# Kernel tuning notes

Measured on AMD Instinct MI355X. Metric: run time of the kernel, lower is better.

## Reference

```python
import jax, jax.numpy as jnp
import numpy as np


def _ln(z, g, b):
    m = z.mean(-1, keepdims=True)
    v = ((z - m) ** 2).mean(-1, keepdims=True)
    return (z - m) * jax.lax.rsqrt(v + 1e-5) * g + b


def _pe(T, D):
    # standard sinusoidal positional encoding (T, D)
    pos = np.arange(T)[:, None]
    i = np.arange(D // 2)[None, :]
    ang = pos / np.power(10000.0, 2.0 * i / D)
    pe = np.zeros((T, D), dtype=np.float32)
    pe[:, 0::2] = np.sin(ang)
    pe[:, 1::2] = np.cos(ang)
    return jnp.asarray(pe)


def _whconv(z, Hinc, filt, W, b):
    # Wavelet hypergraph convolution: psi diag(filt) psi^{-1} Z W + b
    # psi = heat-kernel wavelet of normalized hypergraph Laplacian, 2nd-order Taylor (K=2, s=1)
    S = Hinc.shape[0]
    Dv = Hinc.sum(1) + 1e-6          # node degrees
    De = Hinc.sum(0) + 1e-6          # hyperedge degrees
    Hn = Hinc * (Dv ** -0.5)[:, None]
    A = (Hn / De[None, :]) @ Hn.T    # Dv^-1/2 H De^-1 H^T Dv^-1/2
    I = jnp.eye(S, dtype=z.dtype)
    L = I - A
    L2 = 0.5 * (L @ L)
    psi = I - L + L2                  # exp(-L) approx
    psi_inv = I + L + L2              # exp(+L) approx
    return psi @ (filt[:, None] * (psi_inv @ z)) @ W + b


def setup_inputs():
    S, T, F, D, NS, E, K = 2048, 64, 16, 256, 4, 128, 32
    key = jax.random.key(0)
    ks = iter(jax.random.split(key, 64))
    nrm = lambda shp: jax.random.normal(next(ks), shp, jnp.float32) * 0.02
    return dict(
        x=jax.random.normal(next(ks), (S, T, F), jnp.float32),
        snapshot=(jax.random.uniform(next(ks), (NS, S, E)) < 0.05).astype(jnp.float32),
        params_snapshot=jax.random.uniform(next(ks), (NS,), jnp.float32, 0.0, 0.99),
        beta=jnp.array([0.33, 0.33, 0.33], jnp.float32),
        W_emb=nrm((F, D)), b_emb=jnp.zeros((D,), jnp.float32),
        Wq=nrm((D, D)), bq=jnp.zeros((D,), jnp.float32),
        Wk=nrm((D, D)), bk=jnp.zeros((D,), jnp.float32),
        Wv=nrm((D, D)), bv=jnp.zeros((D,), jnp.float32),
        Wo=nrm((D, D)), bo=jnp.zeros((D,), jnp.float32),
        ln1_g=jnp.ones((D,), jnp.float32), ln1_b=jnp.zeros((D,), jnp.float32),
        W_int=nrm((D, D)), b_int=jnp.zeros((D,), jnp.float32),
        W_mix=nrm((2 * D, D)), b_mix=jnp.zeros((D,), jnp.float32),
        ln2_g=jnp.ones((D,), jnp.float32), ln2_b=jnp.zeros((D,), jnp.float32),
        Wt=nrm((D, D)), bt=jnp.zeros((D,), jnp.float32), vt=nrm((D,)),
        Wh1=nrm((D, D)), bh1=jnp.zeros((D,), jnp.float32), filt1=jnp.ones((S,), jnp.float32),
        Wh2=nrm((D, D)), bh2=jnp.zeros((D,), jnp.float32), filt2=jnp.ones((S,), jnp.float32),
        Wa=nrm((D, D)), Wb=nrm((D, D)), Wg=nrm((D, D)), bg=jnp.zeros((D,), jnp.float32),
        Wm1=nrm((D, D)), bm1=jnp.zeros((D,), jnp.float32),
        Wm2=nrm((D, 1)), bm2=jnp.zeros((1,), jnp.float32),
        num_edges=K,
    )


def reference(x, snapshot, params_snapshot, beta, W_emb, b_emb, Wq, bq, Wk, bk, Wv, bv,
              Wo, bo, ln1_g, ln1_b, W_int, b_int, W_mix, b_mix, ln2_g, ln2_b,
              Wt, bt, vt, Wh1, bh1, filt1, Wh2, bh2, filt2, Wa, Wb, Wg, bg,
              Wm1, bm1, Wm2, bm2, num_edges):
    S, T, _ = x.shape
    D = W_emb.shape[1]
    H = 8
    dh = D // H
    # feature embedding + positional encoding
    h = x @ W_emb + b_emb + _pe(T, D)
    # intra-stock (per-stock temporal) multi-head self-attention + residual + LN
    q = (h @ Wq + bq).reshape(S, T, H, dh)
    k = (h @ Wk + bk).reshape(S, T, H, dh)
    v = (h @ Wv + bv).reshape(S, T, H, dh)
    att = jax.nn.softmax(jnp.einsum('sqhd,skhd->shqk', q, k) / jnp.sqrt(jnp.float32(dh)), axis=-1)
    o = jnp.einsum('shqk,skhd->sqhd', att, v).reshape(S, T, D) @ Wo + bo
    h = _ln(h + o, ln1_g, ln1_b)
    # intensity function + mixing layer (Linear -> ReLU -> LayerNorm)
    intensity = jax.nn.softplus(h @ W_int + b_int)
    z = jax.nn.relu(jnp.concatenate([h, intensity], axis=-1) @ W_mix + b_mix)
    h = _ln(z, ln2_g, ln2_b)
    # temporal attention pooling: (S,T,D) -> (S,D)
    u = jnp.tanh(h @ Wt + bt)
    a = jax.nn.softmax(u @ vt, axis=-1)          # (S,T)
    xs = jnp.einsum('st,std->sd', a, h)           # (S,D)
    # per-snapshot two-layer wavelet hypergraph conv (dropout = eval identity)
    def per_snap(Hinc):
        r1 = jax.nn.leaky_relu(_whconv(xs, Hinc, filt1, Wh1, bh1), 0.1)
        return _whconv(r1, Hinc, filt2, Wh2, bh2)
    reps = jax.vmap(per_snap)(snapshot)           # (NS,S,D)
    hyper = jnp.einsum('n,nsd->sd', params_snapshot, reps)
    # dynamic graph learning: top-k learned similarity graph
    sim = (xs @ Wa) @ (xs @ Wb).T / jnp.sqrt(jnp.float32(D))
    kth = jax.lax.top_k(sim, num_edges)[0][:, -1]
    Adyn = jax.nn.softmax(jnp.where(sim >= kth[:, None], sim, -jnp.inf), axis=-1)
    dyn = jax.nn.relu(Adyn @ xs @ Wg + bg)
    # fusion ('sum' mode) + MLP head
    w = jax.nn.softmax(beta)
    fused = w[0] * xs + w[1] * dyn + w[2] * hyper
    return jax.nn.relu(fused @ Wm1 + bm1) @ Wm2 + bm2   # (S,1)
```

## Files before the change

### kernel.cpp

```cpp
#include <hip/hip_runtime.h>
#include <math.h>

#define S_ 2048
#define T_ 64
#define F_ 16
#define D_ 256
#define NS_ 4
#define E_ 128
#define H_ 8
#define KC_ 32
#define SD_ (S_*D_)
#define HS 260

#define PK_ATT 0
#define PK_WO  393216
#define PK_WI  524288
#define PK_WT  655360
#define PK_WM  786432
#define PKBASE 11674112

typedef __attribute__((ext_vector_type(8))) short bf16x8;
typedef __attribute__((ext_vector_type(4))) float f32x4;

__device__ __forceinline__ float warp_sum64(float v){
  #pragma unroll
  for (int o=32;o>=1;o>>=1) v += __shfl_xor(v,o);
  return v;
}
__device__ __forceinline__ float warp_max64(float v){
  #pragma unroll
  for (int o=32;o>=1;o>>=1) v = fmaxf(v,__shfl_xor(v,o));
  return v;
}
__device__ __forceinline__ float softplus_f(float v){
  return fmaxf(v,0.f) + log1pf(__expf(-fabsf(v)));
}
__device__ __forceinline__ float tanh_f(float v){
  float t = __expf(-2.f*fabsf(v));
  float r = (1.f-t)/(1.f+t);
  return copysignf(r, v);
}
__device__ __forceinline__ void splitf(float f, short& h, short& l){
  unsigned u = __float_as_uint(f);
  unsigned hb = (u + 0x7FFFu + ((u>>16)&1u)) >> 16;
  float fl = f - __uint_as_float(hb<<16);
  unsigned v = __float_as_uint(fl);
  unsigned lb = (v + 0x7FFFu + ((v>>16)&1u)) >> 16;
  h = (short)hb; l = (short)lb;
}
__device__ __forceinline__ f32x4 mfma3(bf16x8 ah, bf16x8 al, bf16x8 bh, bf16x8 bl, f32x4 c){
  c = __builtin_amdgcn_mfma_f32_16x16x32_bf16(al, bh, c, 0,0,0);
  c = __builtin_amdgcn_mfma_f32_16x16x32_bf16(ah, bl, c, 0,0,0);
  c = __builtin_amdgcn_mfma_f32_16x16x32_bf16(ah, bh, c, 0,0,0);
  return c;
}
__device__ __forceinline__ void afrag_f32(const float* base, int stride, int rbase, int ks, int lane, bf16x8& hi, bf16x8& lo){
  const float* p = base + (rbase + (lane&15))*stride + ks + ((lane>>4)<<3);
  #pragma unroll
  for (int jj=0;jj<8;++jj){ short h,l; splitf(p[jj],h,l); hi[jj]=h; lo[jj]=l; }
}
__device__ __forceinline__ void bfrag_pk(const unsigned* pk, int tile, int lane, bf16x8& hi, bf16x8& lo){
  const unsigned* p = pk + (((tile<<6) + lane)<<3);
  #pragma unroll
  for (int jj=0;jj<8;++jj){ unsigned u=p[jj]; hi[jj]=(short)(u & 0xffffu); lo[jj]=(short)(u>>16); }
}

__global__ void pack_qkv(const float* __restrict__ W, short* __restrict__ dst, int vplane){
  int i = blockIdx.x*256 + threadIdx.x;
  int jj=i&7, n=(i>>3)&15, q=(i>>7)&3, ntg=(i>>9)&15, kt=i>>13;
  float f = W[(kt*32 + q*8 + jj)*256 + (ntg*16+n)];
  short h,l; splitf(f,h,l);
  int hp = ntg>>2, ntl = ntg&3;
  int base = ((hp*8+kt)*6 + vplane*2)*2048;
  int local = ntl*512 + (q*16+n)*8 + jj;
  dst[base+local] = h;
  dst[base+2048+local] = l;
}
__global__ void pack_post(const float* __restrict__ W, short* __restrict__ dst){
  int i = blockIdx.x*256 + threadIdx.x;
  int jj=i&7, n=(i>>3)&15, q=(i>>7)&3, ntg=(i>>9)&15, kt=i>>13;
  float f = W[(kt*32 + q*8 + jj)*256 + (ntg*16+n)];
  short h,l; splitf(f,h,l);
  int dl = kt*16384 + ntg*512 + (q*16+n)*8 + jj;
  dst[dl] = h;
  dst[dl+8192] = l;
}

__global__ void pe_kernel(float* __restrict__ pe){
  int i = blockIdx.x*256 + threadIdx.x;
  int t = i >> 8, d = i & 255;
  int ii = d >> 1;
  float w = __expf(-(float)ii * (logf(10000.f)/128.f));
  float ang = (float)t * w;
  pe[i] = (d & 1) ? cosf(ang) : sinf(ang);
}

__launch_bounds__(512,1)
__global__ void stageA_kernel(
    const float* __restrict__ x, const float* __restrict__ pe,
    const float* __restrict__ Wemb, const float* __restrict__ bemb,
    const float* __restrict__ bq, const float* __restrict__ bk, const float* __restrict__ bv,
    const float* __restrict__ bo,
    const float* __restrict__ ln1g, const float* __restrict__ ln1b,
    const float* __restrict__ bint,
    const float* __restrict__ bmix,
    const float* __restrict__ ln2g, const float* __restrict__ ln2b,
    const float* __restrict__ bt,
    const float* __restrict__ vt,
    const short* __restrict__ pkc,
    float* __restrict__ xs)
{
  __shared__ float hbuf[T_][HS];
  __shared__ __attribute__((aligned(16))) char smem[85504];

  short*    wst   = (short*)smem;
  unsigned* k2f2  = (unsigned*)smem;
  unsigned* v2f2  = (unsigned*)(smem + 16384);
  float*    qb2   = (float*)(smem + 32768);
  float*    scb2  = (float*)(smem + 50176);
  float*    smallb= (float*)(smem + 84992);

  const int j  = threadIdx.x;
  const int s  = blockIdx.x;
  const int w  = j >> 6;
  const int lane = j & 63;
  const int m_ = lane & 15, qd = lane >> 4;
  const int rg2 = w >> 1, par = w & 1;
  const int rbase = rg2*16;
  const int rv = w*8;
  const int c0 = lane;

  {
    float* xb = (float*)smem;
    const float* xp = x + (long)s*T_*F_;
    for (int i=j; i<T_*F_; i+=512) xb[i] = xp[i];
  }
  __syncthreads();

  {
    const float* xb = (const float*)smem;
    float acc[8][4];
    #pragma unroll
    for (int r=0;r<8;++r){acc[r][0]=0;acc[r][1]=0;acc[r][2]=0;acc[r][3]=0;}
    #pragma unroll
    for (int k=0;k<F_;++k){
      float w0=Wemb[k*D_+c0], w1=Wemb[k*D_+c0+64], w2=Wemb[k*D_+c0+128], w3=Wemb[k*D_+c0+192];
      #pragma unroll
      for (int r=0;r<8;++r){
        float hv = xb[(rv+r)*F_+k];
        acc[r][0]+=hv*w0; acc[r][1]+=hv*w1; acc[r][2]+=hv*w2; acc[r][3]+=hv*w3;
      }
    }
    float b0=bemb[c0],b1=bemb[c0+64],b2=bemb[c0+128],b3=bemb[c0+192];
    #pragma unroll
    for (int r=0;r<8;++r){
      int t = rv+r;
      hbuf[t][c0]     = acc[r][0]+b0+pe[t*D_+c0];
      hbuf[t][c0+64]  = acc[r][1]+b1+pe[t*D_+c0+64];
      hbuf[t][c0+128] = acc[r][2]+b2+pe[t*D_+c0+128];
      hbuf[t][c0+192] = acc[r][3]+b3+pe[t*D_+c0+192];
    }
  }
  __syncthreads();

  bf16x8 AH[8], AL[8];
  #pragma unroll
  for (int kt=0;kt<8;++kt) afrag_f32(&hbuf[0][0], HS, rbase, kt*32, lane, AH[kt], AL[kt]);

  const float rs = 0.17677669529663687f;
  f32x4 co[8];
  #pragma unroll
  for (int t=0;t<8;++t) co[t] = (f32x4){0.f,0.f,0.f,0.f};

  for (int hp=0; hp<4; ++hp){
    f32x4 qa[2],ka[2],va[2];
    #pragma unroll
    for (int t=0;t<2;++t){
      qa[t]=(f32x4){0.f,0.f,0.f,0.f};
      ka[t]=(f32x4){0.f,0.f,0.f,0.f};
      va[t]=(f32x4){0.f,0.f,0.f,0.f};
    }
    bf16x8 pre[3];
    {
      const short* b0 = pkc + PK_ATT + (hp*8)*12288;
      #pragma unroll
      for (int r=0;r<3;++r) pre[r] = *(const bf16x8*)(b0 + (j+r*512)*8);
    }
    for (int kt=0; kt<8; ++kt){
      __syncthreads();
      #pragma unroll
      for (int r=0;r<3;++r) *(bf16x8*)(wst + (j+r*512)*8) = pre[r];
      __syncthreads();
      if (kt<7){
        const short* nb = pkc + PK_ATT + (hp*8+kt+1)*12288;
        #pragma unroll
        for (int r=0;r<3;++r) pre[r] = *(const bf16x8*)(nb + (j+r*512)*8);
      }
      bf16x8 ah = AH[kt], al = AL[kt];
      #pragma unroll
      for (int t=0;t<2;++t){
        int ntl = par*2+t;
        bf16x8 bh,bl;
        bh = *(bf16x8*)(wst +         ntl*512 + lane*8);
        bl = *(bf16x8*)(wst + 2048  + ntl*512 + lane*8);
        qa[t]=mfma3(ah,al,bh,bl,qa[t]);
        bh = *(bf16x8*)(wst + 4096  + ntl*512 + lane*8);
        bl = *(bf16x8*)(wst + 6144  + ntl*512 + lane*8);
        ka[t]=mfma3(ah,al,bh,bl,ka[t]);
        bh = *(bf16x8*)(wst + 8192  + ntl*512 + lane*8);
        bl = *(bf16x8*)(wst + 10240 + ntl*512 + lane*8);
        va[t]=mfma3(ah,al,bh,bl,va[t]);
      }
    }
    __syncthreads();
    #pragma unroll
    for (int t=0;t<2;++t){
      int ntg = par*2+t;
      #pragma unroll
      for (int r=0;r<4;++r){
        int trow = rbase + qd*4 + r;
        int pcp = ntg*16 + m_;
        int head = pcp >> 5;
        int cp = pcp & 31;
        int col = hp*64 + pcp;
        qb2[trow*68 + pcp] = (qa[t][r] + bq[col]) * rs;
        short hS,lS;
        float kv2 = ka[t][r] + bk[col];
        splitf(kv2,hS,lS);
        k2f2[head*2048 + (((trow>>4)*4 + (cp>>3))*16 + (trow&15))*8 + (cp&7)]
            = (unsigned)(unsigned short)hS | ((unsigned)(unsigned short)lS<<16);
        float vv2 = va[t][r] + bv[col];
        splitf(vv2,hS,lS);
        v2f2[head*2048 + ((((trow>>5)*2 + (cp>>4))*4 + ((trow>>3)&3))*16 + (cp&15))*8 + (trow&7)]
            = (unsigned)(unsigned short)hS | ((unsigned)(unsigned short)lS<<16);
      }
    }
    __syncthreads();
    float* scb = scb2 + par*4352;
    {
      bf16x8 ah,al;
      afrag_f32(qb2, 68, rbase, par*32, lane, ah, al);
      f32x4 sc4[4];
      #pragma unroll
      for (int nt=0;nt<4;++nt){
        bf16x8 bh,bl; bfrag_pk(k2f2 + par*2048, nt, lane, bh, bl);
        sc4[nt] = mfma3(ah,al,bh,bl,(f32x4){0.f,0.f,0.f,0.f});
      }
      #pragma unroll
      for (int r=0;r<4;++r){
        float mx = fmaxf(fmaxf(sc4[0][r],sc4[1][r]),fmaxf(sc4[2][r],sc4[3][r]));
        #pragma unroll
        for (int o=8;o>=1;o>>=1) mx = fmaxf(mx, __shfl_xor(mx,o));
        float es = 0.f;
        #pragma unroll
        for (int nt=0;nt<4;++nt){ float e=__expf(sc4[nt][r]-mx); sc4[nt][r]=e; es+=e; }
        #pragma unroll
        for (int o=8;o>=1;o>>=1) es += __shfl_xor(es,o);
        float inv = 1.f/es;
        int trow = rbase + qd*4 + r;
        #pragma unroll
        for (int nt=0;nt<4;++nt) scb[trow*68 + nt*16 + m_] = sc4[nt][r]*inv;
      }
    }
    {
      f32x4 oa[2];
      oa[0]=(f32x4){0.f,0.f,0.f,0.f}; oa[1]=(f32x4){0.f,0.f,0.f,0.f};
      #pragma unroll
      for (int kt=0;kt<2;++kt){
        bf16x8 ah2,al2; afrag_f32(scb, 68, rbase, kt*32, lane, ah2, al2);
        #pragma unroll
        for (int nt=0;nt<2;++nt){
          bf16x8 bh,bl; bfrag_pk(v2f2 + par*2048, kt*2+nt, lane, bh, bl);
          oa[nt]=mfma3(ah2,al2,bh,bl,oa[nt]);
        }
      }
      #pragma unroll
      for (int nt=0;nt<2;++nt){
        #pragma unroll
        for (int r=0;r<4;++r)
          qb2[(rbase+qd*4+r)*68 + par*32 + nt*16 + m_] = oa[nt][r];
      }
    }
    for (int ks=0; ks<2; ++ks){
      bf16x8 preo[4];
      {
        const short* wob = pkc + PK_WO + (hp*2+ks)*16384;
        #pragma unroll
        for (int r=0;r<4;++r) preo[r] = *(const bf16x8*)(wob + (j+r*512)*8);
      }
      __syncthreads();
      #pragma unroll
      for (int r=0;r<4;++r) *(bf16x8*)(wst + (j+r*512)*8) = preo[r];
      __syncthreads();
      bf16x8 ah,al; afrag_f32(qb2, 68, rbase, ks*32, lane, ah, al);
      #pragma unroll
      for (int t=0;t<8;++t){
        int ntg = 2*t+par;
        bf16x8 bh = *(bf16x8*)(wst +        ntg*512 + lane*8);
        bf16x8 bl = *(bf16x8*)(wst + 8192 + ntg*512 + lane*8);
        co[t]=mfma3(ah,al,bh,bl,co[t]);
      }
    }
  }

  #pragma unroll
  for (int t=0;t<8;++t){
    int cc = (2*t+par)*16+m_;
    float bov = bo[cc];
    #pragma unroll
    for (int r=0;r<4;++r)
      hbuf[rbase+qd*4+r][cc] += co[t][r] + bov;
  }
  __syncthreads();

  {
    float g0=ln1g[c0],g1=ln1g[c0+64],g2=ln1g[c0+128],g3=ln1g[c0+192];
    float bb0=ln1b[c0],bb1=ln1b[c0+64],bb2=ln1b[c0+128],bb3=ln1b[c0+192];
    for (int rr=0;rr<8;++rr){
      int t=rv+rr;
      float v0=hbuf[t][c0],v1=hbuf[t][c0+64],v2=hbuf[t][c0+128],v3=hbuf[t][c0+192];
      float sm=warp_sum64(v0+v1+v2+v3);
      float sq=warp_sum64(v0*v0+v1*v1+v2*v2+v3*v3);
      float mean=sm*(1.f/256.f);
      float inv=rsqrtf(fmaxf(sq*(1.f/256.f)-mean*mean,0.f)+1e-5f);
      hbuf[t][c0]    =(v0-mean)*inv*g0+bb0;
      hbuf[t][c0+64] =(v1-mean)*inv*g1+bb1;
      hbuf[t][c0+128]=(v2-mean)*inv*g2+bb2;
      hbuf[t][c0+192]=(v3-mean)*inv*g3+bb3;
    }
  }
  __syncthreads();

  f32x4 az[8];
  #pragma unroll
  for (int t=0;t<8;++t) az[t]=(f32x4){0.f,0.f,0.f,0.f};
  {
    bf16x8 prew[4];
    #pragma unroll
    for (int r=0;r<4;++r) prew[r] = *(const bf16x8*)(pkc + PK_WM + (j+r*512)*8);
    for (int kt=0; kt<8; ++kt){
      __syncthreads();
      #pragma unroll
      for (int r=0;r<4;++r) *(bf16x8*)(wst + (j+r*512)*8) = prew[r];
      __syncthreads();
      if (kt<7){
        const short* nb = pkc + PK_WM + (kt+1)*16384;
        #pragma unroll
        for (int r=0;r<4;++r) prew[r] = *(const bf16x8*)(nb + (j+r*512)*8);
      }
      bf16x8 ah,al; afrag_f32(&hbuf[0][0], HS, rbase, kt*32, lane, ah, al);
      #pragma unroll
      for (int t=0;t<8;++t){
        int ntg = 2*t+par;
        bf16x8 bh = *(bf16x8*)(wst +        ntg*512 + lane*8);
        bf16x8 bl = *(bf16x8*)(wst + 8192 + ntg*512 + lane*8);
        az[t]=mfma3(ah,al,bh,bl,az[t]);
      }
    }
  }

  {
    f32x4 ai[8];
    #pragma unroll
    for (int t=0;t<8;++t) ai[t]=(f32x4){0.f,0.f,0.f,0.f};
    bf16x8 prew[4];
    #pragma unroll
    for (int r=0;r<4;++r) prew[r] = *(const bf16x8*)(pkc + PK_WI + (j+r*512)*8);
    for (int kt=0; kt<8; ++kt){
      __syncthreads();
      #pragma unroll
      for (int r=0;r<4;++r) *(bf16x8*)(wst + (j+r*512)*8) = prew[r];
      __syncthreads();
      if (kt<7){
        const short* nb = pkc + PK_WI + (kt+1)*16384;
        #pragma unroll
        for (int r=0;r<4;++r) prew[r] = *(const bf16x8*)(nb + (j+r*512)*8);
      }
      bf16x8 ah,al; afrag_f32(&hbuf[0][0], HS, rbase, kt*32, lane, ah, al);
      #pragma unroll
      for (int t=0;t<8;++t){
        int ntg = 2*t+par;
        bf16x8 bh = *(bf16x8*)(wst +        ntg*512 + lane*8);
        bf16x8 bl = *(bf16x8*)(wst + 8192 + ntg*512 + lane*8);
        ai[t]=mfma3(ah,al,bh,bl,ai[t]);
      }
    }
    __syncthreads();
    #pragma unroll
    for (int t=0;t<8;++t){
      int cc = (2*t+par)*16+m_;
      float bb = bint[cc];
      #pragma unroll
      for (int r=0;r<4;++r)
        hbuf[rbase+qd*4+r][cc] = softplus_f(ai[t][r]+bb);
    }
  }

  {
    bf16x8 prew[4];
    #pragma unroll
    for (int r=0;r<4;++r) prew[r] = *(const bf16x8*)(pkc + PK_WM + 8*16384 + (j+r*512)*8);
    for (int kt=0; kt<8; ++kt){
      __syncthreads();
      #pragma unroll
      for (int r=0;r<4;++r) *(bf16x8*)(wst + (j+r*512)*8) = prew[r];
      __syncthreads();
      if (kt<7){
        const short* nb = pkc + PK_WM + (9+kt)*16384;
        #pragma unroll
        for (int r=0;r<4;++r) prew[r] = *(const bf16x8*)(nb + (j+r*512)*8);
      }
      bf16x8 ah,al; afrag_f32(&hbuf[0][0], HS, rbase, kt*32, lane, ah, al);
      #pragma unroll
      for (int t=0;t<8;++t){
        int ntg = 2*t+par;
        bf16x8 bh = *(bf16x8*)(wst +        ntg*512 + lane*8);
        bf16x8 bl = *(bf16x8*)(wst + 8192 + ntg*512 + lane*8);
        az[t]=mfma3(ah,al,bh,bl,az[t]);
      }
    }
  }
  __syncthreads();
  #pragma unroll
  for (int t=0;t<8;++t){
    int cc = (2*t+par)*16+m_;
    float bb = bmix[cc];
    #pragma unroll
    for (int r=0;r<4;++r)
      hbuf[rbase+qd*4+r][cc] = fmaxf(az[t][r]+bb,0.f);
  }
  __syncthreads();

  {
    float g0=ln2g[c0],g1=ln2g[c0+64],g2=ln2g[c0+128],g3=ln2g[c0+192];
    float bb0=ln2b[c0],bb1=ln2b[c0+64],bb2=ln2b[c0+128],bb3=ln2b[c0+192];
    for (int rr=0;rr<8;++rr){
      int t=rv+rr;
      float v0=hbuf[t][c0],v1=hbuf[t][c0+64],v2=hbuf[t][c0+128],v3=hbuf[t][c0+192];
      float sm=warp_sum64(v0+v1+v2+v3);
      float sq=warp_sum64(v0*v0+v1*v1+v2*v2+v3*v3);
      float mean=sm*(1.f/256.f);
      float inv=rsqrtf(fmaxf(sq*(1.f/256.f)-mean*mean,0.f)+1e-5f);
      hbuf[t][c0]    =(v0-mean)*inv*g0+bb0;
      hbuf[t][c0+64] =(v1-mean)*inv*g1+bb1;
      hbuf[t][c0+128]=(v2-mean)*inv*g2+bb2;
      hbuf[t][c0+192]=(v3-mean)*inv*g3+bb3;
    }
  }

  {
    f32x4 at4[8];
    #pragma unroll
    for (int t=0;t<8;++t) at4[t]=(f32x4){0.f,0.f,0.f,0.f};
    bf16x8 prew[4];
    #pragma unroll
    for (int r=0;r<4;++r) prew[r] = *(const bf16x8*)(pkc + PK_WT + (j+r*512)*8);
    for (int kt=0; kt<8; ++kt){
      __syncthreads();
      #pragma unroll
      for (int r=0;r<4;++r) *(bf16x8*)(wst + (j+r*512)*8) = prew[r];
      __syncthreads();
      if (kt<7){
        const short* nb = pkc + PK_WT + (kt+1)*16384;
        #pragma unroll
        for (int r=0;r<4;++r) prew[r] = *(const bf16x8*)(nb + (j+r*512)*8);
      }
      bf16x8 ah,al; afrag_f32(&hbuf[0][0], HS, rbase, kt*32, lane, ah, al);
      #pragma unroll
      for (int t=0;t<8;++t){
        int ntg = 2*t+par;
        bf16x8 bh = *(bf16x8*)(wst +        ntg*512 + lane*8);
        bf16x8 bl = *(bf16x8*)(wst + 8192 + ntg*512 + lane*8);
        at4[t]=mfma3(ah,al,bh,bl,at4[t]);
      }
    }
    float pr[4] = {0.f,0.f,0.f,0.f};
    #pragma unroll
    for (int t=0;t<8;++t){
      int cc = (2*t+par)*16+m_;
      float btc = bt[cc], vtc = vt[cc];
      #pragma unroll
      for (int r=0;r<4;++r) pr[r] += tanh_f(at4[t][r]+btc)*vtc;
    }
    #pragma unroll
    for (int r=0;r<4;++r){
      float p = pr[r];
      p += __shfl_xor(p,1); p += __shfl_xor(p,2);
      p += __shfl_xor(p,4); p += __shfl_xor(p,8);
      if (m_==0) smallb[par*64 + rbase + qd*4 + r] = p;
    }
  }
  __syncthreads();
  if (j < 64){
    float v = smallb[j] + smallb[64+j];
    float m = warp_max64(v);
    float e = __expf(v-m);
    float ssum = warp_sum64(e);
    smallb[64+j] = e/ssum;
  }
  __syncthreads();
  if (j < 256){
    float acc=0.f;
    #pragma unroll 8
    for (int t=0;t<T_;++t) acc += smallb[64+t]*hbuf[t][j];
    xs[(long)s*D_+j] = acc;
  }
}

__global__ void hg_deg(const float* __restrict__ Hinc, float* __restrict__ Dv, float* __restrict__ De){
  const int n = blockIdx.y, s0 = blockIdx.x*64;
  const float* Hp = Hinc + (long)n*S_*E_;
  const int j = threadIdx.x;
  {
    int r = j>>2, q = j&3;
    const float* rp = Hp + (long)(s0+r)*E_ + q*32;
    float sm=0;
    #pragma unroll
    for (int e=0;e<32;++e) sm += rp[e];
    sm += __shfl_xor(sm,1); sm += __shfl_xor(sm,2);
    if (q==0) Dv[n*S_+s0+r]=sm+1e-6f;
  }
  if (j < E_){
    float cs=0;
    for (int ss=0;ss<64;++ss) cs += Hp[(long)(s0+ss)*E_+j];
    atomicAdd(&De[n*E_+j], cs);
  }
}

__global__ void hg_scale(const float* __restrict__ Hinc, const float* __restrict__ Dv,
                         const float* __restrict__ De, float* __restrict__ Hn, float* __restrict__ HnD){
  long i = (long)blockIdx.x*256+threadIdx.x;
  int n = (int)(i >> 18);
  int rem = (int)(i & 262143);
  int srow = rem >> 7;
  int e = rem & 127;
  float h = Hinc[i];
  float hn = h * rsqrtf(Dv[n*S_+srow]);
  Hn[i] = hn;
  HnD[i] = hn / (De[n*E_+e]+1e-6f);
}

__launch_bounds__(256,1)
__global__ void hg_phase1(const float* __restrict__ Hn, const float* __restrict__ M,
                          long mz, float* __restrict__ Ppart)
{
  __shared__ float hl[64*E_];
  __shared__ float ml[64*128];
  const int kc = blockIdx.x, dh = blockIdx.y, n = blockIdx.z;
  const int j = threadIdx.x;
  const float* Hp = Hn + ((long)n*S_ + (long)kc*64)*E_;
  const float* Mp = M + (long)n*mz + (long)kc*64*D_ + dh*128;
  for (int i=j*4; i<64*E_; i+=1024) *(float4*)&hl[i] = *(const float4*)&Hp[i];
  for (int i=j*4; i<64*128; i+=1024){
    int row = i>>7, cc = i&127;
    *(float4*)&ml[i] = *(const float4*)&Mp[(long)row*D_ + cc];
  }
  __syncthreads();
  const int eg = j & 15, dg = j >> 4;
  float acc[8][8];
  #pragma unroll
  for (int e=0;e<8;++e){
    #pragma unroll
    for (int d=0;d<8;++d) acc[e][d]=0.f;
  }
  for (int ss=0; ss<64; ++ss){
    float hv[8], mv[8];
    *(float4*)&hv[0] = *(const float4*)&hl[ss*E_+eg*8];
    *(float4*)&hv[4] = *(const float4*)&hl[ss*E_+eg*8+4];
    *(float4*)&mv[0] = *(const float4*)&ml[ss*128+dg*8];
    *(float4*)&mv[4] = *(const float4*)&ml[ss*128+dg*8+4];
    #pragma unroll
    for (int e=0;e<8;++e){
      #pragma unroll
      for (int d=0;d<8;++d) acc[e][d] += hv[e]*mv[d];
    }
  }
  float* Pp = Ppart + (long)(n*KC_+kc)*E_*D_ + dh*128;
  #pragma unroll
  for (int e=0;e<8;++e){
    int erow = eg*8+e;
    #pragma unroll
    for (int d4=0;d4<8;d4+=4){
      float4 v = make_float4(acc[e][d4],acc[e][d4+1],acc[e][d4+2],acc[e][d4+3]);
      *(float4*)&Pp[(long)erow*D_ + dg*8 + d4] = v;
    }
  }
}

__global__ void hg_reduceP(const float* __restrict__ Ppart, float* __restrict__ P){
  const int n = blockIdx.y;
  int base = blockIdx.x*1024;
  for (int i = base + threadIdx.x; i < base+1024; i += 256){
    const float* pp = Ppart + (long)n*KC_*E_*D_ + i;
    float a = 0;
    #pragma unroll
    for (int kc=0;kc<KC_;++kc) a += pp[(long)kc*E_*D_];
    P[(long)n*E_*D_ + i] = a;
  }
}

__launch_bounds__(256,1)
__global__ void hg_phase2(const float* __restrict__ HnD, const float* __restrict__ P,
                          const float* __restrict__ X1, long x1z, float c1,
                          const float* __restrict__ X2, long x2z, float c2,
                          float c3, const float* __restrict__ filt, int usefilt,
                          float* __restrict__ out)
{
  __shared__ float al[E_*68];
  __shared__ float pl[E_*68];
  const int st = blockIdx.x*64, dt = blockIdx.y*64, n = blockIdx.z;
  const int j = threadIdx.x;
  {
    const int r = j >> 2, k0 = (j&3)*32;
    const float* hp = HnD + ((long)n*S_ + st + r)*E_ + k0;
    #pragma unroll
    for (int kk=0; kk<32; kk+=4){
      float4 v = *(const float4*)&hp[kk];
      al[(k0+kk+0)*68+r]=v.x;
      al[(k0+kk+1)*68+r]=v.y;
      al[(k0+kk+2)*68+r]=v.z;
      al[(k0+kk+3)*68+r]=v.w;
    }
  }
  for (int idx=j; idx<E_*16; idx+=256){
    int k = idx>>4, dsub = (idx&15)*4;
    *(float4*)&pl[k*68+dsub] = *(const float4*)&P[((long)n*E_+k)*D_ + dt + dsub];
  }
  __syncthreads();
  const int tx = j&15, ty = j>>4;
  float acc[4][4];
  #pragma unroll
  for (int i=0;i<4;++i){acc[i][0]=0;acc[i][1]=0;acc[i][2]=0;acc[i][3]=0;}
  for (int k=0;k<E_;++k){
    float4 a = *(const float4*)&al[k*68+ty*4];
    float4 b = *(const float4*)&pl[k*68+tx*4];
    acc[0][0]+=a.x*b.x; acc[0][1]+=a.x*b.y; acc[0][2]+=a.x*b.z; acc[0][3]+=a.x*b.w;
    acc[1][0]+=a.y*b.x; acc[1][1]+=a.y*b.y; acc[1][2]+=a.y*b.z; acc[1][3]+=a.y*b.w;
    acc[2][0]+=a.z*b.x; acc[2][1]+=a.z*b.y; acc[2][2]+=a.z*b.z; acc[2][3]+=a.z*b.w;
    acc[3][0]+=a.w*b.x; acc[3][1]+=a.w*b.y; acc[3][2]+=a.w*b.z; acc[3][3]+=a.w*b.w;
  }
  #pragma unroll
  for (int i=0;i<4;++i){
    int srow = st + ty*4 + i;
    float f = usefilt ? filt[srow] : 1.f;
    #pragma unroll
    for (int m=0;m<4;++m){
      int d = dt + tx*4+m;
      long li = (long)srow*D_ + d;
      float v = c3*acc[i][m];
      if (X1) v += c1*X1[x1z*n + li];
      if (X2) v += c2*X2[x2z*n + li];
      out[((long)n*S_ + srow)*D_ + d] = f*v;
    }
  }
}

__launch_bounds__(256,1)
__global__ void gemm_nn(const float* __restrict__ A, long az,
                        const float* __restrict__ B, long bz,
                        float* __restrict__ C, long cz,
                        int K, int N,
                        const float* __restrict__ bias, int act)
{
  __shared__ float al[32*68];
  __shared__ float bl[32*68];
  const int mt = blockIdx.x*64, nt = blockIdx.y*64, zz = blockIdx.z;
  const int j = threadIdx.x;
  const float* Ap = A + (long)az*zz;
  const float* Bp = B + (long)bz*zz;
  const int tx = j&15, ty = j>>4;
  float acc[4][4];
  #pragma unroll
  for (int i=0;i<4;++i){acc[i][0]=0;acc[i][1]=0;acc[i][2]=0;acc[i][3]=0;}
  for (int k0=0;k0<K;k0+=32){
    #pragma unroll
    for (int half=0; half<2; ++half){
      int idx = j + half*256;
      int r = idx>>3, kk=(idx&7)*4;
      float4 v = *(const float4*)&Ap[(long)(mt+r)*K + k0+kk];
      al[(kk+0)*68+r]=v.x; al[(kk+1)*68+r]=v.y; al[(kk+2)*68+r]=v.z; al[(kk+3)*68+r]=v.w;
    }
    #pragma unroll
    for (int half=0; half<2; ++half){
      int idx = j + half*256;
      int r = idx>>4, cc=(idx&15)*4;
      *(float4*)&bl[r*68+cc] = *(const float4*)&Bp[(long)(k0+r)*N + nt+cc];
    }
    __syncthreads();
    #pragma unroll
    for (int kk=0;kk<32;++kk){
      float4 a = *(const float4*)&al[kk*68+ty*4];
      float4 b = *(const float4*)&bl[kk*68+tx*4];
      acc[0][0]+=a.x*b.x; acc[0][1]+=a.x*b.y; acc[0][2]+=a.x*b.z; acc[0][3]+=a.x*b.w;
      acc[1][0]+=a.y*b.x; acc[1][1]+=a.y*b.y; acc[1][2]+=a.y*b.z; acc[1][3]+=a.y*b.w;
      acc[2][0]+=a.z*b.x; acc[2][1]+=a.z*b.y; acc[2][2]+=a.z*b.z; acc[2][3]+=a.z*b.w;
      acc[3][0]+=a.w*b.x; acc[3][1]+=a.w*b.y; acc[3][2]+=a.w*b.z; acc[3][3]+=a.w*b.w;
    }
    __syncthreads();
  }
  #pragma unroll
  for (int i=0;i<4;++i){
    int row = mt+ty*4+i;
    #pragma unroll
    for (int m=0;m<4;++m){
      int col = nt+tx*4+m;
      float v = acc[i][m];
      if (bias) v += bias[col];
      if (act==1) v = fmaxf(v,0.f);
      else if (act==2) v = (v>0.f)? v : 0.1f*v;
      C[(long)cz*zz + (long)row*N + col] = v;
    }
  }
}

__launch_bounds__(256,1)
__global__ void gemm_nt_scaled(const float* __restrict__ A, const float* __restrict__ B,
                               float* __restrict__ C, int K, float scale)
{
  __shared__ float al[32*68];
  __shared__ float bl[32*68];
  const int mt = blockIdx.x*64, nt = blockIdx.y*64;
  const int j = threadIdx.x;
  const int tx = j&15, ty = j>>4;
  float acc[4][4];
  #pragma unroll
  for (int i=0;i<4;++i){acc[i][0]=0;acc[i][1]=0;acc[i][2]=0;acc[i][3]=0;}
  for (int k0=0;k0<K;k0+=32){
    #pragma unroll
    for (int half=0; half<2; ++half){
      int idx = j + half*256;
      int r = idx>>3, kk=(idx&7)*4;
      float4 v = *(const float4*)&A[(long)(mt+r)*K + k0+kk];
      al[(kk+0)*68+r]=v.x; al[(kk+1)*68+r]=v.y; al[(kk+2)*68+r]=v.z; al[(kk+3)*68+r]=v.w;
    }
    #pragma unroll
    for (int half=0; half<2; ++half){
      int idx = j + half*256;
      int r = idx>>3, kk=(idx&7)*4;
      float4 v = *(const float4*)&B[(long)(nt+r)*K + k0+kk];
      bl[(kk+0)*68+r]=v.x; bl[(kk+1)*68+r]=v.y; bl[(kk+2)*68+r]=v.z; bl[(kk+3)*68+r]=v.w;
    }
    __syncthreads();
    #pragma unroll
    for (int kk=0;kk<32;++kk){
      float4 a = *(const float4*)&al[kk*68+ty*4];
      float4 b = *(const float4*)&bl[kk*68+tx*4];
      acc[0][0]+=a.x*b.x; acc[0][1]+=a.x*b.y; acc[0][2]+=a.x*b.z; acc[0][3]+=a.x*b.w;
      acc[1][0]+=a.y*b.x; acc[1][1]+=a.y*b.y; acc[1][2]+=a.y*b.z; acc[1][3]+=a.y*b.w;
      acc[2][0]+=a.z*b.x; acc[2][1]+=a.z*b.y; acc[2][2]+=a.z*b.z; acc[2][3]+=a.z*b.w;
      acc[3][0]+=a.w*b.x; acc[3][1]+=a.w*b.y; acc[3][2]+=a.w*b.z; acc[3][3]+=a.w*b.w;
    }
    __syncthreads();
  }
  #pragma unroll
  for (int i=0;i<4;++i){
    #pragma unroll
    for (int m=0;m<4;++m){
      C[(long)(mt+ty*4+i)*S_ + nt+tx*4+m] = acc[i][m]*scale;
    }
  }
}

__launch_bounds__(256,1)
__global__ void topk_gather(const float* __restrict__ sim, const float* __restrict__ xs,
                            const int* __restrict__ Kp, float* __restrict__ dynpre)
{
  __shared__ float row[S_];
  __shared__ float work[S_];
  __shared__ float wred[4]; __shared__ int ired[4];
  __shared__ float selw[256]; __shared__ int seli[256];
  __shared__ int cnt; __shared__ float sh_kth, sh_max, sh_den;
  const int s = blockIdx.x, j = threadIdx.x;
  const float* rp = sim + (long)s*S_;
  for (int i=j;i<S_;i+=256){ float v=rp[i]; row[i]=v; work[i]=v; }
  if (j==0) cnt=0;
  __syncthreads();
  const int K = Kp[0];
  for (int it=0; it<K; ++it){
    float m=-3.0e38f; int mi=0;
    for (int i=j;i<S_;i+=256){ float v=work[i]; if (v>m){m=v;mi=i;} }
    #pragma unroll
    for (int o=32;o>=1;o>>=1){
      float om=__shfl_xor(m,o); int oi=__shfl_xor(mi,o);
      if (om>m){m=om;mi=oi;}
    }
    if ((j&63)==0){ wred[j>>6]=m; ired[j>>6]=mi; }
    __syncthreads();
    if (j==0){
      float bm=wred[0]; int bi=ired[0];
      #pragma unroll
      for (int w=1;w<4;++w) if (wred[w]>bm){bm=wred[w];bi=ired[w];}
      work[bi]=-3.0e38f;
      if (it==0) sh_max=bm;
      sh_kth=bm;
    }
    __syncthreads();
  }
  const float kth=sh_kth, rmax=sh_max;
  for (int i=j;i<S_;i+=256){
    float v=row[i];
    if (v>=kth){
      int p=atomicAdd(&cnt,1);
      if (p<256){ seli[p]=i; selw[p]=__expf(v-rmax); }
    }
  }
  __syncthreads();
  int c = cnt; if (c>256) c=256;
// ... 147 lines not shown
```

Measured before the change: 1.459 ms.

## Store activations as split bf16 planes and stream weights directly from global

The activation buffer moves from fp32 in LDS to pre-split hi/lo bf16 planes, so MFMA A-fragments become single vector loads instead of per-element splitting. The post-LN GEMMs are restructured so each wave owns two output column tiles across all 64 rows, with B fragments loaded straight from global memory and register double-buffered across the W_mix, W_int and W_t GEMMs. This removes the per-k-step LDS weight staging and its two barriers, and the Wo GEMM also reads weights directly from global. The cost is more global/L2 traffic per wave and a split/recombine step on every elementwise read-modify-write of activations, with a small precision change from the double-bf16 storage.

```diff
diff --git a/kernel.cpp b/kernel.cpp
--- a/kernel.cpp
+++ b/kernel.cpp
@@ -10,7 +10,7 @@
 #define H_ 8
 #define KC_ 32
 #define SD_ (S_*D_)
-#define HS 260
+#define PS 264
 
 #define PK_ATT 0
 #define PK_WO  393216
@@ -59,10 +59,22 @@
   #pragma unroll
   for (int jj=0;jj<8;++jj){ short h,l; splitf(p[jj],h,l); hi[jj]=h; lo[jj]=l; }
 }
+__device__ __forceinline__ bf16x8 afrag_pk(const short* plane, int rbase, int ks, int lane){
+  return *(const bf16x8*)(plane + (rbase + (lane&15))*PS + ks + ((lane>>4)<<3));
+}
 __device__ __forceinline__ void bfrag_pk(const unsigned* pk, int tile, int lane, bf16x8& hi, bf16x8& lo){
   const unsigned* p = pk + (((tile<<6) + lane)<<3);
   #pragma unroll
   for (int jj=0;jj<8;++jj){ unsigned u=p[jj]; hi[jj]=(short)(u & 0xffffu); lo[jj]=(short)(u>>16); }
+}
+__device__ __forceinline__ void store_h(short* Hh, short* Hl, int r, int c, float f){
+  short h,l; splitf(f,h,l);
+  Hh[r*PS+c]=h; Hl[r*PS+c]=l;
+}
+__device__ __forceinline__ float load_h(const short* Hh, const short* Hl, int r, int c){
+  int idx=r*PS+c;
+  return __uint_as_float(((unsigned)(unsigned short)Hh[idx])<<16)
+       + __uint_as_float(((unsigned)(unsigned short)Hl[idx])<<16);
 }
 
 __global__ void pack_qkv(const float* __restrict__ W, short* __restrict__ dst, int vplane){
@@ -110,7 +122,8 @@
     const short* __restrict__ pkc,
     float* __restrict__ xs)
 {
-  __shared__ float hbuf[T_][HS];
+  __shared__ __attribute__((aligned(16))) short hbh[64*PS];
+  __shared__ __attribute__((aligned(16))) short hbl[64*PS];
   __shared__ __attribute__((aligned(16))) char smem[85504];
 
   short*    wst   = (short*)smem;
@@ -118,7 +131,7 @@
   unsigned* v2f2  = (unsigned*)(smem + 16384);
   float*    qb2   = (float*)(smem + 32768);
   float*    scb2  = (float*)(smem + 50176);
-  float*    smallb= (float*)(smem + 84992);
+  float*    poolb = (float*)smem;
 
   const int j  = threadIdx.x;
   const int s  = blockIdx.x;
@@ -152,20 +165,24 @@
       }
     }
     float b0=bemb[c0],b1=bemb[c0+64],b2=bemb[c0+128],b3=bemb[c0+192];
+    __syncthreads();
     #pragma unroll
     for (int r=0;r<8;++r){
       int t = rv+r;
-      hbuf[t][c0]     = acc[r][0]+b0+pe[t*D_+c0];
-      hbuf[t][c0+64]  = acc[r][1]+b1+pe[t*D_+c0+64];
-      hbuf[t][c0+128] = acc[r][2]+b2+pe[t*D_+c0+128];
-      hbuf[t][c0+192] = acc[r][3]+b3+pe[t*D_+c0+192];
+      store_h(hbh,hbl,t,c0,     acc[r][0]+b0+pe[t*D_+c0]);
+      store_h(hbh,hbl,t,c0+64,  acc[r][1]+b1+pe[t*D_+c0+64]);
+      store_h(hbh,hbl,t,c0+128, acc[r][2]+b2+pe[t*D_+c0+128]);
+      store_h(hbh,hbl,t,c0+192, acc[r][3]+b3+pe[t*D_+c0+192]);
     }
   }
   __syncthreads();
 
   bf16x8 AH[8], AL[8];
   #pragma unroll
-  for (int kt=0;kt<8;++kt) afrag_f32(&hbuf[0][0], HS, rbase, kt*32, lane, AH[kt], AL[kt]);
+  for (int kt=0;kt<8;++kt){
+    AH[kt] = afrag_pk(hbh, rbase, kt*32, lane);
+    AL[kt] = afrag_pk(hbl, rbase, kt*32, lane);
+  }
 
   const float rs = 0.17677669529663687f;
   f32x4 co[8];
@@ -281,23 +298,15 @@
           qb2[(rbase+qd*4+r)*68 + par*32 + nt*16 + m_] = oa[nt][r];
       }
     }
+    __syncthreads();
     for (int ks=0; ks<2; ++ks){
-      bf16x8 preo[4];
-      {
-        const short* wob = pkc + PK_WO + (hp*2+ks)*16384;
-        #pragma unroll
-        for (int r=0;r<4;++r) preo[r] = *(const bf16x8*)(wob + (j+r*512)*8);
-      }
-      __syncthreads();
-      #pragma unroll
-      for (int r=0;r<4;++r) *(bf16x8*)(wst + (j+r*512)*8) = preo[r];
-      __syncthreads();
       bf16x8 ah,al; afrag_f32(qb2, 68, rbase, ks*32, lane, ah, al);
+      const short* wob = pkc + PK_WO + (hp*2+ks)*16384 + lane*8;
       #pragma unroll
       for (int t=0;t<8;++t){
         int ntg = 2*t+par;
-        bf16x8 bh = *(bf16x8*)(wst +        ntg*512 + lane*8);
-        bf16x8 bl = *(bf16x8*)(wst + 8192 + ntg*512 + lane*8);
+        bf16x8 bh = *(const bf16x8*)(wob + ntg*512);
+        bf16x8 bl = *(const bf16x8*)(wob + 8192 + ntg*512);
         co[t]=mfma3(ah,al,bh,bl,co[t]);
       }
     }
@@ -308,8 +317,10 @@
     int cc = (2*t+par)*16+m_;
     float bov = bo[cc];
     #pragma unroll
-    for (int r=0;r<4;++r)
-      hbuf[rbase+qd*4+r][cc] += co[t][r] + bov;
+    for (int r=0;r<4;++r){
+      int row = rbase+qd*4+r;
+      store_h(hbh,hbl,row,cc, load_h(hbh,hbl,row,cc) + co[t][r] + bov);
+    }
   }
   __syncthreads();
 
@@ -318,191 +329,169 @@
     float bb0=ln1b[c0],bb1=ln1b[c0+64],bb2=ln1b[c0+128],bb3=ln1b[c0+192];
     for (int rr=0;rr<8;++rr){
       int t=rv+rr;
-      float v0=hbuf[t][c0],v1=hbuf[t][c0+64],v2=hbuf[t][c0+128],v3=hbuf[t][c0+192];
+      float v0=load_h(hbh,hbl,t,c0),    v1=load_h(hbh,hbl,t,c0+64);
+      float v2=load_h(hbh,hbl,t,c0+128),v3=load_h(hbh,hbl,t,c0+192);
       float sm=warp_sum64(v0+v1+v2+v3);
       float sq=warp_sum64(v0*v0+v1*v1+v2*v2+v3*v3);
       float mean=sm*(1.f/256.f);
       float inv=rsqrtf(fmaxf(sq*(1.f/256.f)-mean*mean,0.f)+1e-5f);
-      hbuf[t][c0]    =(v0-mean)*inv*g0+bb0;
-      hbuf[t][c0+64] =(v1-mean)*inv*g1+bb1;
-      hbuf[t][c0+128]=(v2-mean)*inv*g2+bb2;
-      hbuf[t][c0+192]=(v3-mean)*inv*g3+bb3;
-    }
-  }
-  __syncthreads();
-
-  f32x4 az[8];
-  #pragma unroll
-  for (int t=0;t<8;++t) az[t]=(f32x4){0.f,0.f,0.f,0.f};
-  {
-    bf16x8 prew[4];
-    #pragma unroll
-    for (int r=0;r<4;++r) prew[r] = *(const bf16x8*)(pkc + PK_WM + (j+r*512)*8);
-    for (int kt=0; kt<8; ++kt){
-      __syncthreads();
-      #pragma unroll
-      for (int r=0;r<4;++r) *(bf16x8*)(wst + (j+r*512)*8) = prew[r];
-      __syncthreads();
-      if (kt<7){
-        const short* nb = pkc + PK_WM + (kt+1)*16384;
-        #pragma unroll
-        for (int r=0;r<4;++r) prew[r] = *(const bf16x8*)(nb + (j+r*512)*8);
-      }
-      bf16x8 ah,al; afrag_f32(&hbuf[0][0], HS, rbase, kt*32, lane, ah, al);
-      #pragma unroll
-      for (int t=0;t<8;++t){
-        int ntg = 2*t+par;
-        bf16x8 bh = *(bf16x8*)(wst +        ntg*512 + lane*8);
-        bf16x8 bl = *(bf16x8*)(wst + 8192 + ntg*512 + lane*8);
-        az[t]=mfma3(ah,al,bh,bl,az[t]);
-      }
-    }
-  }
-
-  {
-    f32x4 ai[8];
-    #pragma unroll
-    for (int t=0;t<8;++t) ai[t]=(f32x4){0.f,0.f,0.f,0.f};
-    bf16x8 prew[4];
-    #pragma unroll
-    for (int r=0;r<4;++r) prew[r] = *(const bf16x8*)(pkc + PK_WI + (j+r*512)*8);
-    for (int kt=0; kt<8; ++kt){
-      __syncthreads();
-      #pragma unroll
-      for (int r=0;r<4;++r) *(bf16x8*)(wst + (j+r*512)*8) = prew[r];
-      __syncthreads();
-      if (kt<7){
-        const short* nb = pkc + PK_WI + (kt+1)*16384;
-        #pragma unroll
-        for (int r=0;r<4;++r) prew[r] = *(const bf16x8*)(nb + (j+r*512)*8);
-      }
-      bf16x8 ah,al; afrag_f32(&hbuf[0][0], HS, rbase, kt*32, lane, ah, al);
-      #pragma unroll
-      for (int t=0;t<8;++t){
-        int ntg = 2*t+par;
-        bf16x8 bh = *(bf16x8*)(wst +        ntg*512 + lane*8);
-        bf16x8 bl = *(bf16x8*)(wst + 8192 + ntg*512 + lane*8);
-        ai[t]=mfma3(ah,al,bh,bl,ai[t]);
-      }
-    }
-    __syncthreads();
-    #pragma unroll
-    for (int t=0;t<8;++t){
-      int cc = (2*t+par)*16+m_;
-      float bb = bint[cc];
+      store_h(hbh,hbl,t,c0,    (v0-mean)*inv*g0+bb0);
+      store_h(hbh,hbl,t,c0+64, (v1-mean)*inv*g1+bb1);
+      store_h(hbh,hbl,t,c0+128,(v2-mean)*inv*g2+bb2);
+      store_h(hbh,hbl,t,c0+192,(v3-mean)*inv*g3+bb3);
+    }
+  }
+  __syncthreads();
+
+  auto loadB=[&](bf16x8* d, const short* base, int kt){
+    const short* p = base + kt*16384 + lane*8;
+    d[0]=*(const bf16x8*)(p + (2*w)*512);
+    d[1]=*(const bf16x8*)(p + 8192 + (2*w)*512);
+    d[2]=*(const bf16x8*)(p + (2*w+1)*512);
+    d[3]=*(const bf16x8*)(p + 8192 + (2*w+1)*512);
+  };
+  const short* BM = pkc + PK_WM;
+  const short* BI = pkc + PK_WI;
+  const short* BT = pkc + PK_WT;
+
+  f32x4 az[4][2], ai[4][2];
+  #pragma unroll
+  for (int rt=0;rt<4;++rt){
+    az[rt][0]=(f32x4){0.f,0.f,0.f,0.f}; az[rt][1]=(f32x4){0.f,0.f,0.f,0.f};
+    ai[rt][0]=(f32x4){0.f,0.f,0.f,0.f}; ai[rt][1]=(f32x4){0.f,0.f,0.f,0.f};
+  }
+  bf16x8 cb[4], nb[4];
+  loadB(cb, BM, 0);
+  for (int kt=0; kt<8; ++kt){
+    if (kt<7) loadB(nb, BM, kt+1); else loadB(nb, BI, 0);
+    #pragma unroll
+    for (int rt=0;rt<4;++rt){
+      bf16x8 ah = afrag_pk(hbh, rt*16, kt*32, lane);
+      bf16x8 al = afrag_pk(hbl, rt*16, kt*32, lane);
+      az[rt][0]=mfma3(ah,al,cb[0],cb[1],az[rt][0]);
+      az[rt][1]=mfma3(ah,al,cb[2],cb[3],az[rt][1]);
+    }
+    #pragma unroll
+    for (int r=0;r<4;++r) cb[r]=nb[r];
+  }
+  for (int kt=0; kt<8; ++kt){
+    if (kt<7) loadB(nb, BI, kt+1); else loadB(nb, BM, 8);
+    #pragma unroll
+    for (int rt=0;rt<4;++rt){
+      bf16x8 ah = afrag_pk(hbh, rt*16, kt*32, lane);
+      bf16x8 al = afrag_pk(hbl, rt*16, kt*32, lane);
+      ai[rt][0]=mfma3(ah,al,cb[0],cb[1],ai[rt][0]);
+      ai[rt][1]=mfma3(ah,al,cb[2],cb[3],ai[rt][1]);
+    }
+    #pragma unroll
+    for (int r=0;r<4;++r) cb[r]=nb[r];
+  }
+  __syncthreads();
+  #pragma unroll
+  for (int rt=0;rt<4;++rt){
+    #pragma unroll
+    for (int t=0;t<2;++t){
+      int col=(2*w+t)*16+m_;
+      float bb=bint[col];
       #pragma unroll
       for (int r=0;r<4;++r)
-        hbuf[rbase+qd*4+r][cc] = softplus_f(ai[t][r]+bb);
-    }
-  }
-
-  {
-    bf16x8 prew[4];
-    #pragma unroll
-    for (int r=0;r<4;++r) prew[r] = *(const bf16x8*)(pkc + PK_WM + 8*16384 + (j+r*512)*8);
-    for (int kt=0; kt<8; ++kt){
-      __syncthreads();
-      #pragma unroll
-      for (int r=0;r<4;++r) *(bf16x8*)(wst + (j+r*512)*8) = prew[r];
-      __syncthreads();
-      if (kt<7){
-        const short* nb = pkc + PK_WM + (9+kt)*16384;
-        #pragma unroll
-        for (int r=0;r<4;++r) prew[r] = *(const bf16x8*)(nb + (j+r*512)*8);
-      }
-      bf16x8 ah,al; afrag_f32(&hbuf[0][0], HS, rbase, kt*32, lane, ah, al);
-      #pragma unroll
-      for (int t=0;t<8;++t){
-        int ntg = 2*t+par;
-        bf16x8 bh = *(bf16x8*)(wst +        ntg*512 + lane*8);
-        bf16x8 bl = *(bf16x8*)(wst + 8192 + ntg*512 + lane*8);
-        az[t]=mfma3(ah,al,bh,bl,az[t]);
-      }
-    }
-  }
-  __syncthreads();
-  #pragma unroll
-  for (int t=0;t<8;++t){
-    int cc = (2*t+par)*16+m_;
-    float bb = bmix[cc];
-    #pragma unroll
-    for (int r=0;r<4;++r)
-      hbuf[rbase+qd*4+r][cc] = fmaxf(az[t][r]+bb,0.f);
-  }
-  __syncthreads();
-
+        store_h(hbh,hbl, rt*16+qd*4+r, col, softplus_f(ai[rt][t][r]+bb));
+    }
+  }
+  __syncthreads();
+  for (int kt=0; kt<8; ++kt){
+    if (kt<7) loadB(nb, BM, kt+9); else loadB(nb, BT, 0);
+    #pragma unroll
+    for (int rt=0;rt<4;++rt){
+      bf16x8 ah = afrag_pk(hbh, rt*16, kt*32, lane);
+      bf16x8 al = afrag_pk(hbl, rt*16, kt*32, lane);
+      az[rt][0]=mfma3(ah,al,cb[0],cb[1],az[rt][0]);
+      az[rt][1]=mfma3(ah,al,cb[2],cb[3],az[rt][1]);
+    }
+    #pragma unroll
+    for (int r=0;r<4;++r) cb[r]=nb[r];
+  }
+  __syncthreads();
+  #pragma unroll
+  for (int rt=0;rt<4;++rt){
+    #pragma unroll
+    for (int t=0;t<2;++t){
+      int col=(2*w+t)*16+m_;
+      float bb=bmix[col];
+      #pragma unroll
+      for (int r=0;r<4;++r)
+        store_h(hbh,hbl, rt*16+qd*4+r, col, fmaxf(az[rt][t][r]+bb,0.f));
+    }
+  }
+  __syncthreads();
   {
     float g0=ln2g[c0],g1=ln2g[c0+64],g2=ln2g[c0+128],g3=ln2g[c0+192];
     float bb0=ln2b[c0],bb1=ln2b[c0+64],bb2=ln2b[c0+128],bb3=ln2b[c0+192];
     for (int rr=0;rr<8;++rr){
       int t=rv+rr;
-      float v0=hbuf[t][c0],v1=hbuf[t][c0+64],v2=hbuf[t][c0+128],v3=hbuf[t][c0+192];
+      float v0=load_h(hbh,hbl,t,c0),    v1=load_h(hbh,hbl,t,c0+64);
+      float v2=load_h(hbh,hbl,t,c0+128),v3=load_h(hbh,hbl,t,c0+192);
       float sm=warp_sum64(v0+v1+v2+v3);
       float sq=warp_sum64(v0*v0+v1*v1+v2*v2+v3*v3);
       float mean=sm*(1.f/256.f);
       float inv=rsqrtf(fmaxf(sq*(1.f/256.f)-mean*mean,0.f)+1e-5f);
-      hbuf[t][c0]    =(v0-mean)*inv*g0+bb0;
-      hbuf[t][c0+64] =(v1-mean)*inv*g1+bb1;
-      hbuf[t][c0+128]=(v2-mean)*inv*g2+bb2;
-      hbuf[t][c0+192]=(v3-mean)*inv*g3+bb3;
-    }
-  }
-
+      store_h(hbh,hbl,t,c0,    (v0-mean)*inv*g0+bb0);
+      store_h(hbh,hbl,t,c0+64, (v1-mean)*inv*g1+bb1);
+      store_h(hbh,hbl,t,c0+128,(v2-mean)*inv*g2+bb2);
+      store_h(hbh,hbl,t,c0+192,(v3-mean)*inv*g3+bb3);
+    }
+  }
+  __syncthreads();
   {
-    f32x4 at4[8];
-    #pragma unroll
-    for (int t=0;t<8;++t) at4[t]=(f32x4){0.f,0.f,0.f,0.f};
-    bf16x8 prew[4];
-    #pragma unroll
-    for (int r=0;r<4;++r) prew[r] = *(const bf16x8*)(pkc + PK_WT + (j+r*512)*8);
+    f32x4 at4[4][2];
+    #pragma unroll
+    for (int rt=0;rt<4;++rt){
+      at4[rt][0]=(f32x4){0.f,0.f,0.f,0.f}; at4[rt][1]=(f32x4){0.f,0.f,0.f,0.f};
+    }
     for (int kt=0; kt<8; ++kt){
-      __syncthreads();
-      #pragma unroll
-      for (int r=0;r<4;++r) *(bf16x8*)(wst + (j+r*512)*8) = prew[r];
-      __syncthreads();
-      if (kt<7){
-        const short* nb = pkc + PK_WT + (kt+1)*16384;
+      if (kt<7) loadB(nb, BT, kt+1);
+      #pragma unroll
+      for (int rt=0;rt<4;++rt){
+        bf16x8 ah = afrag_pk(hbh, rt*16, kt*32, lane);
+        bf16x8 al = afrag_pk(hbl, rt*16, kt*32, lane);
+        at4[rt][0]=mfma3(ah,al,cb[0],cb[1],at4[rt][0]);
+        at4[rt][1]=mfma3(ah,al,cb[2],cb[3],at4[rt][1]);
+      }
+      #pragma unroll
+      for (int r=0;r<4;++r) cb[r]=nb[r];
+    }
+    #pragma unroll
+    for (int rt=0;rt<4;++rt){
+      #pragma unroll
+      for (int r=0;r<4;++r){
+        int row = rt*16+qd*4+r;
+        float p = 0.f;
         #pragma unroll
-        for (int r=0;r<4;++r) prew[r] = *(const bf16x8*)(nb + (j+r*512)*8);
-      }
-      bf16x8 ah,al; afrag_f32(&hbuf[0][0], HS, rbase, kt*32, lane, ah, al);
-      #pragma unroll
-      for (int t=0;t<8;++t){
-        int ntg = 2*t+par;
-        bf16x8 bh = *(bf16x8*)(wst +        ntg*512 + lane*8);
-        bf16x8 bl = *(bf16x8*)(wst + 8192 + ntg*512 + lane*8);
-        at4[t]=mfma3(ah,al,bh,bl,at4[t]);
-      }
-    }
-    float pr[4] = {0.f,0.f,0.f,0.f};
-    #pragma unroll
-    for (int t=0;t<8;++t){
-      int cc = (2*t+par)*16+m_;
-      float btc = bt[cc], vtc = vt[cc];
-      #pragma unroll
-      for (int r=0;r<4;++r) pr[r] += tanh_f(at4[t][r]+btc)*vtc;
-    }
-    #pragma unroll
-    for (int r=0;r<4;++r){
-      float p = pr[r];
-      p += __shfl_xor(p,1); p += __shfl_xor(p,2);
-      p += __shfl_xor(p,4); p += __shfl_xor(p,8);
-      if (m_==0) smallb[par*64 + rbase + qd*4 + r] = p;
+        for (int t=0;t<2;++t){
+          int col=(2*w+t)*16+m_;
+          p += tanh_f(at4[rt][t][r]+bt[col])*vt[col];
+        }
+        p += __shfl_xor(p,1); p += __shfl_xor(p,2);
+        p += __shfl_xor(p,4); p += __shfl_xor(p,8);
+        if (m_==0) poolb[w*64+row] = p;
+      }
     }
   }
   __syncthreads();
   if (j < 64){
-    float v = smallb[j] + smallb[64+j];
+    float v = 0.f;
+    #pragma unroll
+    for (int ww=0;ww<8;++ww) v += poolb[ww*64+j];
     float m = warp_max64(v);
     float e = __expf(v-m);
     float ssum = warp_sum64(e);
-    smallb[64+j] = e/ssum;
+    poolb[512+j] = e/ssum;
   }
   __syncthreads();
   if (j < 256){
     float acc=0.f;
     #pragma unroll 8
-    for (int t=0;t<T_;++t) acc += smallb[64+t]*hbuf[t][j];
+    for (int t=0;t<T_;++t) acc += poolb[512+t]*load_h(hbh,hbl,t,j);
     xs[(long)s*D_+j] = acc;
   }
 }
```

Result: no change. 1.485 ms (+1.7%).
